# Kernel optimization log

Hardware: AMD Instinct MI355X
Metric: run time of the kernel (lower is better)

Reference implementation:

```python
import jax, jax.numpy as jnp
import numpy as np

# opt hyperparameters
_S, _M, _N_PILOT, _K, _L, _DECAY = 6, 64, 1, 16, 8, 4.0
_N, _P = 4096, 4
_SMK = (_S + 1) * (_M + _N_PILOT + _K)  # 567


def _conv_full(a, b):
    # a: (B, L), b: (B, S) -> (B, S+L-1) full convolution per batch row
    return jax.vmap(lambda u, v: jnp.convolve(u, v, mode='full'))(a, b)


def setup_inputs() -> dict:
    key = jax.random.key(0)
    k1, k2 = jax.random.split(key)
    x = jax.random.normal(k1, (_N, _P, _SMK, 2), dtype=jnp.float32)
    # exponential power-delay profile, normalized (as in __init__/sample)
    power = jnp.exp(-jnp.arange(_L, dtype=jnp.float32) / _DECAY)
    power = power / jnp.sum(power)
    cof = jnp.sqrt(power / 2.0)[None, None, :, None] * jax.random.normal(
        k2, (_N, _P, _L, 2), dtype=jnp.float32)
    return {"x": x, "cof": cof, "M": _M}


def reference(x, cof, M):
    # x: (N,P,SMK,2) complex signal (re/im stacked), cof: (N,P,L,2) channel taps
    N, P, SMK, _ = x.shape
    L = cof.shape[2]
    B = N * P
    hr = cof[..., 0].reshape(B, L)
    hi = cof[..., 1].reshape(B, L)
    xr = x[..., 0].reshape(B, SMK)
    xi = x[..., 1].reshape(B, SMK)
    # complex FIR full convolution: out[i] = sum_j h[i-j] * x[j]
    out_r = _conv_full(hr, xr) - _conv_full(hi, xi)
    out_i = _conv_full(hr, xi) + _conv_full(hi, xr)
    out = jnp.stack([out_r, out_i], axis=-1).reshape(N, P, SMK + L - 1, 2)
    # frequency response: FFT of taps zero-padded to M
    cof_true = jnp.pad(cof, ((0, 0), (0, 0), (0, M - L), (0, 0)))
    Hc = jnp.fft.fft(cof_true[..., 0] + 1j * cof_true[..., 1], axis=-1)
    H_true = jnp.stack([Hc.real.astype(x.dtype), Hc.imag.astype(x.dtype)], axis=-1)
    return out, H_true
```

## Files before the change

### kernel.cpp

```cpp
#include <hip/hip_runtime.h>
#include <math.h>


#define B_ROWS 16384
#define SMK    567
#define LTAPS  8
#define OUTLEN 574
#define MFFT   64

__global__ __launch_bounds__(256) void channel_kernel(
    const float2* __restrict__ x,
    const float2* __restrict__ cof,
    float2* __restrict__ out,
    float2* __restrict__ H)
{
    __shared__ float2 xs[OUTLEN + LTAPS - 1];

    const int b   = blockIdx.x;
    const int tid = threadIdx.x;

    const float2* __restrict__ xrow = x + (size_t)b * SMK;

    if (tid < 2 * (LTAPS - 1)) {
        int idx = (tid < LTAPS - 1) ? tid : (OUTLEN + tid - (LTAPS - 1));
        xs[idx] = make_float2(0.0f, 0.0f);
    }
    for (int i = tid; i < SMK; i += 256) {
        xs[i + (LTAPS - 1)] = xrow[i];
    }

    const float2* __restrict__ crow = cof + (size_t)b * LTAPS;
    float2 h[LTAPS];
    #pragma unroll
    for (int j = 0; j < LTAPS; ++j) h[j] = crow[j];

    __syncthreads();

    float2* __restrict__ orow = out + (size_t)b * OUTLEN;
    #pragma unroll
    for (int it = 0; it < 3; ++it) {
        int i = tid + it * 256;
        if (i < OUTLEN) {
            float sr = 0.0f, si = 0.0f;
            #pragma unroll
            for (int j = 0; j < LTAPS; ++j) {
                float2 xv = xs[i - j + (LTAPS - 1)];
                sr = fmaf(h[j].x, xv.x, sr);
                sr = fmaf(-h[j].y, xv.y, sr);
                si = fmaf(h[j].x, xv.y, si);
                si = fmaf(h[j].y, xv.x, si);
            }
            orow[i] = make_float2(sr, si);
        }
    }

    if (tid < MFFT) {
        const int k = tid;
        float accr = 0.0f, acci = 0.0f;
        #pragma unroll
        for (int l = 0; l < LTAPS; ++l) {
            int t = (k * l) & (MFFT - 1);
            float ang = -6.2831853071795864769f * (float)t * (1.0f / (float)MFFT);
            float s, c;
            __sincosf(ang, &s, &c);
            accr = fmaf(h[l].x, c, accr);
            accr = fmaf(-h[l].y, s, accr);
            acci = fmaf(h[l].x, s, acci);
            acci = fmaf(h[l].y, c, acci);
        }
        H[(size_t)b * MFFT + k] = make_float2(accr, acci);
    }
}

extern "C" void kernel_launch(void* const* d_in, const int* in_sizes, int n_in,
                              void* d_out, int out_size, void* d_ws, size_t ws_size,
                              hipStream_t stream) {
    const float2* x   = (const float2*)d_in[0];
    const float2* cof = (const float2*)d_in[1];
    float* outf = (float*)d_out;

    float2* conv_out = (float2*)outf;
    float2* H        = (float2*)(outf + (size_t)B_ROWS * OUTLEN * 2);

    channel_kernel<<<B_ROWS, 256, 0, stream>>>(x, cof, conv_out, H);
}
```

Measured before the change: 29.67 us.

## Split shared input into planar arrays and compute four outputs per thread

Stores the input row in shared memory as separate real and imaginary planes, so each thread loads a 12-sample sliding window with float4 reads and computes four consecutive outputs, writing them with 16-byte stores. This cuts shared-memory reads and store instructions per output. The DFT of the taps moves to a separate wave (threads 192-255) so it runs alongside the convolution waves instead of after them on the same threads. Only 144 threads now do convolution, leaving one wave idle. The kernel is likely memory-bound, so the compute savings may matter little.

```diff
diff --git a/kernel.cpp b/kernel.cpp
--- a/kernel.cpp
+++ b/kernel.cpp
@@ -7,6 +7,7 @@
 #define LTAPS  8
 #define OUTLEN 574
 #define MFFT   64
+#define XL     592
 
 __global__ __launch_bounds__(256) void channel_kernel(
     const float2* __restrict__ x,
@@ -14,19 +15,23 @@
     float2* __restrict__ out,
     float2* __restrict__ H)
 {
-    __shared__ float2 xs[OUTLEN + LTAPS - 1];
+    __shared__ float xr[XL];
+    __shared__ float xi[XL];
 
     const int b   = blockIdx.x;
     const int tid = threadIdx.x;
 
     const float2* __restrict__ xrow = x + (size_t)b * SMK;
 
-    if (tid < 2 * (LTAPS - 1)) {
-        int idx = (tid < LTAPS - 1) ? tid : (OUTLEN + tid - (LTAPS - 1));
-        xs[idx] = make_float2(0.0f, 0.0f);
+    if (tid < 25) {
+        int idx = (tid < 8) ? tid : (SMK + tid);
+        xr[idx] = 0.0f;
+        xi[idx] = 0.0f;
     }
     for (int i = tid; i < SMK; i += 256) {
-        xs[i + (LTAPS - 1)] = xrow[i];
+        float2 v = xrow[i];
+        xr[8 + i] = v.x;
+        xi[8 + i] = v.y;
     }
 
     const float2* __restrict__ crow = cof + (size_t)b * LTAPS;
@@ -36,37 +41,53 @@
 
     __syncthreads();
 
-    float2* __restrict__ orow = out + (size_t)b * OUTLEN;
-    #pragma unroll
-    for (int it = 0; it < 3; ++it) {
-        int i = tid + it * 256;
-        if (i < OUTLEN) {
-            float sr = 0.0f, si = 0.0f;
+    if (tid < 144) {
+        const int i0 = 4 * tid;
+
+        float4 a0 = *(const float4*)&xr[i0];
+        float4 a1 = *(const float4*)&xr[i0 + 4];
+        float4 a2 = *(const float4*)&xr[i0 + 8];
+        float4 c0 = *(const float4*)&xi[i0];
+        float4 c1 = *(const float4*)&xi[i0 + 4];
+        float4 c2 = *(const float4*)&xi[i0 + 8];
+        float wr[12] = {a0.x, a0.y, a0.z, a0.w, a1.x, a1.y, a1.z, a1.w,
+                        a2.x, a2.y, a2.z, a2.w};
+        float wi[12] = {c0.x, c0.y, c0.z, c0.w, c1.x, c1.y, c1.z, c1.w,
+                        c2.x, c2.y, c2.z, c2.w};
+
+        float sr[4] = {0.f, 0.f, 0.f, 0.f};
+        float si[4] = {0.f, 0.f, 0.f, 0.f};
+        #pragma unroll
+        for (int j = 0; j < LTAPS; ++j) {
+            float hr = h[j].x, hi = h[j].y;
             #pragma unroll
-            for (int j = 0; j < LTAPS; ++j) {
-                float2 xv = xs[i - j + (LTAPS - 1)];
-                sr = fmaf(h[j].x, xv.x, sr);
-                sr = fmaf(-h[j].y, xv.y, sr);
-                si = fmaf(h[j].x, xv.y, si);
-                si = fmaf(h[j].y, xv.x, si);
+            for (int p = 0; p < 4; ++p) {
+                float ar = wr[8 + p - j], ai = wi[8 + p - j];
+                sr[p] = fmaf(hr, ar, sr[p]);
+                sr[p] = fmaf(-hi, ai, sr[p]);
+                si[p] = fmaf(hr, ai, si[p]);
+                si[p] = fmaf(hi, ar, si[p]);
             }
-            orow[i] = make_float2(sr, si);
         }
-    }
 
-    if (tid < MFFT) {
-        const int k = tid;
+        float2* __restrict__ orow = out + (size_t)b * OUTLEN;
+        *(float4*)&orow[i0] = make_float4(sr[0], si[0], sr[1], si[1]);
+        if (i0 + 2 < OUTLEN) {
+            *(float4*)&orow[i0 + 2] = make_float4(sr[2], si[2], sr[3], si[3]);
+        }
+    } else if (tid >= 192) {
+        const int k = tid - 192;
         float accr = 0.0f, acci = 0.0f;
         #pragma unroll
         for (int l = 0; l < LTAPS; ++l) {
             int t = (k * l) & (MFFT - 1);
             float ang = -6.2831853071795864769f * (float)t * (1.0f / (float)MFFT);
-            float s, c;
-            __sincosf(ang, &s, &c);
-            accr = fmaf(h[l].x, c, accr);
-            accr = fmaf(-h[l].y, s, accr);
-            acci = fmaf(h[l].x, s, acci);
-            acci = fmaf(h[l].y, c, acci);
+            float sn, cs;
+            __sincosf(ang, &sn, &cs);
+            accr = fmaf(h[l].x, cs, accr);
+            accr = fmaf(-h[l].y, sn, accr);
+            acci = fmaf(h[l].x, sn, acci);
+            acci = fmaf(h[l].y, cs, acci);
         }
         H[(size_t)b * MFFT + k] = make_float2(accr, acci);
     }
```

Result: slower. 31.05 us (+4.6%).

## Flatten FIR into register-tiled threads over all rows and split FFT into separate blocks

Applied to the files above, without the earlier changes.

Replaces the one-block-per-row shared-memory FIR with a flat grid in which each thread computes 4 consecutive outputs of a row from an 11-sample register window loaded straight from global memory. Outputs are written as float4. The DFT of the taps moves into its own dedicated blocks, so no FIR block leaves threads idle and the 64-point work is no longer serialized at the end of every FIR block. The aim is to drop the LDS staging and __syncthreads and remove the idle lanes from 574-of-768 iteration coverage. In exchange, neighbouring threads read overlapping, unaligned global windows that depend on the cache, and each thread reloads the taps.

```diff
diff --git a/kernel.cpp b/kernel.cpp
--- a/kernel.cpp
+++ b/kernel.cpp
@@ -7,6 +7,9 @@
 #define LTAPS  8
 #define OUTLEN 574
 #define MFFT   64
+#define TPR    144
+#define FIRB   9216
+#define HB     4096
 
 __global__ __launch_bounds__(256) void channel_kernel(
     const float2* __restrict__ x,
@@ -14,61 +17,77 @@
     float2* __restrict__ out,
     float2* __restrict__ H)
 {
-    __shared__ float2 xs[OUTLEN + LTAPS - 1];
-
-    const int b   = blockIdx.x;
+    const int gid = blockIdx.x;
     const int tid = threadIdx.x;
 
-    const float2* __restrict__ xrow = x + (size_t)b * SMK;
+    if (gid < FIRB) {
+        const int gt  = gid * 256 + tid;
+        const int row = gt / TPR;
+        const int p   = gt - row * TPR;
+        const int i0  = 4 * p;
 
-    if (tid < 2 * (LTAPS - 1)) {
-        int idx = (tid < LTAPS - 1) ? tid : (OUTLEN + tid - (LTAPS - 1));
-        xs[idx] = make_float2(0.0f, 0.0f);
-    }
-    for (int i = tid; i < SMK; i += 256) {
-        xs[i + (LTAPS - 1)] = xrow[i];
-    }
+        const float2* __restrict__ xrow = x + (size_t)row * SMK;
 
-    const float2* __restrict__ crow = cof + (size_t)b * LTAPS;
-    float2 h[LTAPS];
-    #pragma unroll
-    for (int j = 0; j < LTAPS; ++j) h[j] = crow[j];
+        const float4* __restrict__ c4 = (const float4*)(cof + (size_t)row * LTAPS);
+        float4 h01 = c4[0], h23 = c4[1], h45 = c4[2], h67 = c4[3];
+        float hr[LTAPS] = {h01.x, h01.z, h23.x, h23.z, h45.x, h45.z, h67.x, h67.z};
+        float hi[LTAPS] = {h01.y, h01.w, h23.y, h23.w, h45.y, h45.w, h67.y, h67.w};
 
-    __syncthreads();
+        float2 w[11];
+        if (p >= 2 && p <= 140) {
+            #pragma unroll
+            for (int m = 0; m < 11; ++m) w[m] = xrow[i0 - 7 + m];
+        } else {
+            #pragma unroll
+            for (int m = 0; m < 11; ++m) {
+                int idx = i0 - 7 + m;
+                w[m] = (idx >= 0 && idx < SMK) ? xrow[idx]
+                                               : make_float2(0.0f, 0.0f);
+            }
+        }
 
-    float2* __restrict__ orow = out + (size_t)b * OUTLEN;
-    #pragma unroll
-    for (int it = 0; it < 3; ++it) {
-        int i = tid + it * 256;
-        if (i < OUTLEN) {
-            float sr = 0.0f, si = 0.0f;
+        float sr[4] = {0.f, 0.f, 0.f, 0.f};
+        float si[4] = {0.f, 0.f, 0.f, 0.f};
+        #pragma unroll
+        for (int j = 0; j < LTAPS; ++j) {
             #pragma unroll
-            for (int j = 0; j < LTAPS; ++j) {
-                float2 xv = xs[i - j + (LTAPS - 1)];
-                sr = fmaf(h[j].x, xv.x, sr);
-                sr = fmaf(-h[j].y, xv.y, sr);
-                si = fmaf(h[j].x, xv.y, si);
-                si = fmaf(h[j].y, xv.x, si);
+            for (int q = 0; q < 4; ++q) {
+                float2 xv = w[7 + q - j];
+                sr[q] = fmaf(hr[j], xv.x, sr[q]);
+                sr[q] = fmaf(-hi[j], xv.y, sr[q]);
+                si[q] = fmaf(hr[j], xv.y, si[q]);
+                si[q] = fmaf(hi[j], xv.x, si[q]);
             }
-            orow[i] = make_float2(sr, si);
         }
-    }
 
-    if (tid < MFFT) {
-        const int k = tid;
+        float4* __restrict__ o4 = (float4*)(out + (size_t)row * OUTLEN + i0);
+        o4[0] = make_float4(sr[0], si[0], sr[1], si[1]);
+        if (p < TPR - 1) {
+            o4[1] = make_float4(sr[2], si[2], sr[3], si[3]);
+        }
+    } else {
+        const int ht  = (gid - FIRB) * 256 + tid;
+        const int row = ht >> 6;
+        const int k   = ht & (MFFT - 1);
+
+        const float4* __restrict__ c4 = (const float4*)(cof + (size_t)row * LTAPS);
+        float4 h01 = c4[0], h23 = c4[1], h45 = c4[2], h67 = c4[3];
+        float hr[LTAPS] = {h01.x, h01.z, h23.x, h23.z, h45.x, h45.z, h67.x, h67.z};
+        float hi[LTAPS] = {h01.y, h01.w, h23.y, h23.w, h45.y, h45.w, h67.y, h67.w};
+
         float accr = 0.0f, acci = 0.0f;
         #pragma unroll
         for (int l = 0; l < LTAPS; ++l) {
             int t = (k * l) & (MFFT - 1);
             float ang = -6.2831853071795864769f * (float)t * (1.0f / (float)MFFT);
-            float s, c;
-            __sincosf(ang, &s, &c);
-            accr = fmaf(h[l].x, c, accr);
-            accr = fmaf(-h[l].y, s, accr);
-            acci = fmaf(h[l].x, s, acci);
-            acci = fmaf(h[l].y, c, acci);
+            float sn, cs;
+            __sincosf(ang, &sn, &cs);
+            accr = fmaf(hr[l], cs, accr);
+            accr = fmaf(-hi[l], sn, accr);
+            acci = fmaf(hr[l], sn, acci);
+            acci = fmaf(hi[l], cs, acci);
         }
-        H[(size_t)b * MFFT + k] = make_float2(accr, acci);
+        H[(size_t)row * MFFT + k] = make_float2(accr, acci);
     }
 }
 
@@ -82,5 +101,5 @@
     float2* conv_out = (float2*)outf;
     float2* H        = (float2*)(outf + (size_t)B_ROWS * OUTLEN * 2);
 
-    channel_kernel<<<B_ROWS, 256, 0, stream>>>(x, cof, conv_out, H);
+    channel_kernel<<<FIRB + HB, 256, 0, stream>>>(x, cof, conv_out, H);
 }
```

New measurement: 33.86 us. +14.1%, slower.
